# Kernel tuning notes

Hardware: AMD Instinct MI355X
Metric: run time of the kernel (lower is better)

## Reference

```python
import jax, jax.numpy as jnp
import numpy as np

N = 50000       # nodes
E = 800000      # directed edges (avg degree 16)
DIN, DH, DOUT = 128, 128, 64
NUM_LAYERS = 5


def setup_inputs() -> dict:
    key = jax.random.key(0)
    ks = jax.random.split(key, 2 + 2 * NUM_LAYERS)
    x = jax.random.normal(ks[0], (N, DIN), dtype=jnp.float32)
    edge_index = jax.random.randint(ks[1], (2, E), 0, N, dtype=jnp.int64)
    dims = [(DIN, DH)] + [(DH, DH)] * (NUM_LAYERS - 2) + [(DH, DOUT)]
    inp = {"x": x, "edge_index": edge_index}
    for i, (di, do) in enumerate(dims):
        # PyG Linear weight is [out, in]; glorot-ish scale
        inp[f"W{i}"] = jax.random.normal(ks[2 + 2 * i], (do, di), dtype=jnp.float32) / np.sqrt(di)
        inp[f"b{i}"] = jnp.zeros((do,), dtype=jnp.float32)
    return inp


def gcn_conv(x, W, b, src, dst, n):
    """PyG GCNConv: symmetric normalization with self-loops (already appended)."""
    h = x @ W.T                                   # [N, do]
    ones = jnp.ones(src.shape[0], dtype=h.dtype)
    deg = jax.ops.segment_sum(ones, dst, num_segments=n)          # [N]
    dinv = jnp.where(deg > 0, jax.lax.rsqrt(jnp.maximum(deg, 1.0)), 0.0)
    norm = dinv[src] * dinv[dst]                  # [E+N]
    msg = h[src] * norm[:, None]                  # [E+N, do] gather
    out = jax.ops.segment_sum(msg, dst, num_segments=n)           # scatter-add
    return out + b


def reference(x, edge_index, W0, b0, W1, b1, W2, b2, W3, b3, W4, b4):
    n = x.shape[0]
    loop = jnp.arange(n, dtype=edge_index.dtype)
    src = jnp.concatenate([edge_index[0], loop])  # add self-loops
    dst = jnp.concatenate([edge_index[1], loop])
    Ws = [W0, W1, W2, W3, W4]
    bs = [b0, b1, b2, b3, b4]
    for i in range(NUM_LAYERS):
        x = gcn_conv(x, Ws[i], bs[i], src, dst, n)
        if i != NUM_LAYERS - 1:
            x = jax.nn.relu(x)
            # dropout is identity in eval mode (training=False)
    return x
```

## Files before the change

### kernel.cpp

```cpp
#include <hip/hip_runtime.h>
#include <hip/hip_fp16.h>
#include <math.h>


typedef _Float16 f16x8 __attribute__((ext_vector_type(8)));
typedef float f32x4 __attribute__((ext_vector_type(4)));

#define NBIN 128
#define NB 512
#define WCAP 12288


__global__ __launch_bounds__(256) void k_detect(const int* __restrict__ ei, int* __restrict__ flag, int E) {
  __shared__ int nonzero;
  if (threadIdx.x == 0) nonzero = 0;
  __syncthreads();
  int idx = threadIdx.x;
  if (idx < E && idx < 256) {
    if (ei[2 * idx + 1] != 0) atomicOr(&nonzero, 1);
  }
  __syncthreads();
  if (threadIdx.x == 0) *flag = (nonzero == 0) ? 1 : 0;
}

__device__ __forceinline__ int edge_at(const void* ei, int is64, long long idx) {
  if (is64) return (int)((const long long*)ei)[idx];
  return ((const int*)ei)[idx];
}

__global__ __launch_bounds__(512) void k_cnt2(const void* __restrict__ ei, const int* __restrict__ flag,
                                              int* __restrict__ bcnt, int E, int n, int W) {
  __shared__ int cnt[NBIN];
  int t = threadIdx.x;
  if (t < NBIN) cnt[t] = 0;
  __syncthreads();
  int is64 = *flag;
  int chunk = (E + NB - 1) / NB;
  int base = blockIdx.x * chunk;
  int end = base + chunk;
  if (end > E) end = E;
  for (int i = base + t; i < end; i += 512) {
    int s = edge_at(ei, is64, i);
    int v = edge_at(ei, is64, (long long)E + i);
    if ((unsigned)v < (unsigned)n && (unsigned)s < (unsigned)n) atomicAdd(&cnt[v / W], 1);
  }
  __syncthreads();
  if (t < NBIN) bcnt[blockIdx.x * NBIN + t] = cnt[t];
}

__global__ __launch_bounds__(256) void k_scanb(int* __restrict__ bcnt, int* __restrict__ bintot) {
  __shared__ int buf[NB];
  int bin = blockIdx.x;
  int t = threadIdx.x;
  int a0 = bcnt[(size_t)t * NBIN + bin];
  int a1 = bcnt[(size_t)(t + 256) * NBIN + bin];
  buf[t] = a0;
  buf[t + 256] = a1;
  __syncthreads();
  for (int off = 1; off < NB; off <<= 1) {
    int x0 = (t >= off) ? buf[t - off] : 0;
    int x1 = (t + 256 >= off) ? buf[t + 256 - off] : 0;
    __syncthreads();
    buf[t] += x0;
    buf[t + 256] += x1;
    __syncthreads();
  }
  bcnt[(size_t)t * NBIN + bin] = buf[t] - a0;
  bcnt[(size_t)(t + 256) * NBIN + bin] = buf[t + 256] - a1;
  if (t == 255) bintot[bin] = buf[NB - 1];
}

__global__ __launch_bounds__(64) void k_base2(const int* __restrict__ bintot, int* __restrict__ binbase) {
  if (threadIdx.x == 0) {
    int run = 0;
    for (int i = 0; i < NBIN; ++i) {
      binbase[i] = run;
      run += bintot[i];
    }
    binbase[NBIN] = run;
  }
}

__global__ __launch_bounds__(512) void k_scat(const void* __restrict__ ei, const int* __restrict__ flag,
                                              const int* __restrict__ bcnt, const int* __restrict__ binbase,
                                              uint2* __restrict__ ebin, int E, int n, int W) {
  __shared__ int cur[NBIN];
  int t = threadIdx.x;
  if (t < NBIN) cur[t] = binbase[t] + bcnt[blockIdx.x * NBIN + t];
  __syncthreads();
  int is64 = *flag;
  int chunk = (E + NB - 1) / NB;
  int base = blockIdx.x * chunk;
  int end = base + chunk;
  if (end > E) end = E;
  for (int i = base + t; i < end; i += 512) {
    int s = edge_at(ei, is64, i);
    int v = edge_at(ei, is64, (long long)E + i);
    if ((unsigned)v < (unsigned)n && (unsigned)s < (unsigned)n) {
      int pos = atomicAdd(&cur[v / W], 1);
      ebin[pos] = make_uint2((unsigned)s, (unsigned)v);
    }
  }
}

__global__ __launch_bounds__(256) void k_build(const uint2* __restrict__ ebin, const int* __restrict__ binbase,
                                               int* __restrict__ row_ptr, float* __restrict__ dinv,
                                               int* __restrict__ col, int n, int W) {
  __shared__ int hist[512];
  __shared__ int scanBuf[512];
  __shared__ unsigned int win[WCAP];
  int t = threadIdx.x;
  int b = blockIdx.x;
  int v0 = b * W;
  int v1 = v0 + W;
  if (v1 > n) v1 = n;
  int nloc = v1 - v0;
  if (nloc <= 0) {
    if (b == NBIN - 1 && t == 0) row_ptr[n] = binbase[NBIN];
    return;
  }
  int ebase = binbase[b];
  int ecnt = binbase[b + 1] - ebase;

  for (int i = t; i < 512; i += 256) { hist[i] = 0; scanBuf[i] = 0; }
  __syncthreads();
  for (int j = t; j < ecnt; j += 256) {
    uint2 e = ebin[ebase + j];
    atomicAdd(&hist[(int)e.y - v0], 1);
  }
  __syncthreads();
  for (int i = t; i < nloc; i += 256) {
    scanBuf[i] = hist[i];
    dinv[v0 + i] = 1.0f / sqrtf((float)(hist[i] + 1));
  }
  __syncthreads();
  int i1 = t, i2 = t + 256;
  for (int off = 1; off < 512; off <<= 1) {
    int a = (i1 >= off) ? scanBuf[i1 - off] : 0;
    int c = (i2 >= off) ? scanBuf[i2 - off] : 0;
    __syncthreads();
    scanBuf[i1] += a;
    scanBuf[i2] += c;
    __syncthreads();
  }
  for (int i = t; i < nloc; i += 256) row_ptr[v0 + i] = ebase + scanBuf[i] - hist[i];
  if (b == NBIN - 1 && t == 0) row_ptr[n] = ebase + ecnt;
  __syncthreads();
  for (int i = t; i < nloc; i += 256) hist[i] = scanBuf[i] - hist[i];
  __syncthreads();
  if (ecnt <= WCAP) {
    for (int j = t; j < ecnt; j += 256) {
      uint2 e = ebin[ebase + j];
      int pos = atomicAdd(&hist[(int)e.y - v0], 1);
      win[pos] = e.x;
    }
    __syncthreads();
    for (int j = t; j < ecnt; j += 256) col[ebase + j] = (int)win[j];
  } else {
    for (int j = t; j < ecnt; j += 256) {
      uint2 e = ebin[ebase + j];
      int pos = atomicAdd(&hist[(int)e.y - v0], 1);
      col[ebase + pos] = (int)e.x;
    }
  }
}


__global__ __launch_bounds__(256) void k_split_x(const float* __restrict__ X, unsigned int* __restrict__ Xh,
                                                 unsigned int* __restrict__ Xr, int n2) {
  int i = blockIdx.x * 256 + threadIdx.x;
  if (i >= n2) return;
  float2 v = ((const float2*)X)[i];
  __half hx = __float2half(v.x), hy = __float2half(v.y);
  float rx = v.x - __half2float(hx), ry = v.y - __half2float(hy);
  __half rxh = __float2half(rx), ryh = __float2half(ry);
  unsigned int ph = ((unsigned int)*(unsigned short*)&hy << 16) | *(unsigned short*)&hx;
  unsigned int pr = ((unsigned int)*(unsigned short*)&ryh << 16) | *(unsigned short*)&rxh;
  Xh[i] = ph;
  Xr[i] = pr;
}

__global__ __launch_bounds__(256) void k_split_w(const float* __restrict__ W, unsigned short* __restrict__ Wh,
                                                 unsigned short* __restrict__ Wr, int cnt) {
  int i = blockIdx.x * 256 + threadIdx.x;
  if (i >= cnt) return;
  float v = W[i];
  __half h = __float2half(v);
  float r = v - __half2float(h);
  __half rh = __float2half(r);
  Wh[i] = *(unsigned short*)&h;
  Wr[i] = *(unsigned short*)&rh;
}


template <int DO>
__global__ __launch_bounds__(256) void gemm_mfma(const unsigned short* __restrict__ Xh,
                                                 const unsigned short* __restrict__ Xr,
                                                 const unsigned short* __restrict__ Wh,
                                                 const unsigned short* __restrict__ Wr,
                                                 const float* __restrict__ dinv, __half* __restrict__ G, int n) {
  constexpr int NCG = DO / 16;
  __shared__ unsigned short sWh[DO * 128];
  __shared__ unsigned short sWr[DO * 128];
  const int tid = threadIdx.x;

#pragma unroll
  for (int it = 0; it < DO / 16; ++it) {
    int t = it * 256 + tid;
    int row = t >> 4, ch = t & 15;
    int sch = ch ^ (row & 7);
    const uint4* gh = (const uint4*)&Wh[(size_t)t * 8];
    const uint4* gr = (const uint4*)&Wr[(size_t)t * 8];
    *(uint4*)&sWh[row * 128 + sch * 8] = *gh;
    *(uint4*)&sWr[row * 128 + sch * 8] = *gr;
  }

  const int wv = tid >> 6;
  const int l = tid & 63;
  const int m = l & 15;
  const int ks = l >> 4;
  const int gr0 = blockIdx.x * 64 + wv * 16;
  const int arow = gr0 + m;

  f16x8 ah[4], ar[4];
  const f16x8 z8 = {0, 0, 0, 0, 0, 0, 0, 0};
#pragma unroll
  for (int kb = 0; kb < 4; ++kb) {
    int koff = kb * 32 + ks * 8;
    if (arow < n) {
      ah[kb] = *(const f16x8*)&Xh[(size_t)arow * 128 + koff];
      ar[kb] = *(const f16x8*)&Xr[(size_t)arow * 128 + koff];
    } else {
      ah[kb] = z8;
      ar[kb] = z8;
    }
  }

  f32x4 acc[NCG];
#pragma unroll
  for (int c = 0; c < NCG; ++c) acc[c] = {0.f, 0.f, 0.f, 0.f};

  __syncthreads();

#pragma unroll
  for (int kb = 0; kb < 4; ++kb) {
    int ch = (kb * 4 + ks) ^ (m & 7);
#pragma unroll
    for (int c = 0; c < NCG; ++c) {
      int brow = c * 16 + m;
      f16x8 bh = *(const f16x8*)&sWh[brow * 128 + ch * 8];
      f16x8 br = *(const f16x8*)&sWr[brow * 128 + ch * 8];
      acc[c] = __builtin_amdgcn_mfma_f32_16x16x32_f16(ah[kb], bh, acc[c], 0, 0, 0);
      acc[c] = __builtin_amdgcn_mfma_f32_16x16x32_f16(ah[kb], br, acc[c], 0, 0, 0);
      acc[c] = __builtin_amdgcn_mfma_f32_16x16x32_f16(ar[kb], bh, acc[c], 0, 0, 0);
    }
  }

  int r0 = gr0 + ks * 4;
  float dv[4];
#pragma unroll
  for (int i = 0; i < 4; ++i) dv[i] = (r0 + i < n) ? dinv[r0 + i] : 0.f;
#pragma unroll
  for (int c = 0; c < NCG; ++c) {
#pragma unroll
    for (int i = 0; i < 4; ++i) {
      int row = r0 + i;
      if (row < n) G[(size_t)row * DO + c * 16 + m] = __float2half(dv[i] * acc[c][i]);
    }
  }
}


__device__ __forceinline__ float2 h2f(unsigned int u) {
  __half2 h = *(__half2*)&u;
  return __half22float2(h);
}

__global__ __launch_bounds__(256) void aggregate128(const unsigned int* __restrict__ G, const float* __restrict__ dinv,
                                                    const float* __restrict__ bias, const int* __restrict__ rp,
                                                    const int* __restrict__ col, unsigned int* __restrict__ Yh,
                                                    unsigned int* __restrict__ Yr, int n) {
  int v = (int)((blockIdx.x * 256 + threadIdx.x) >> 6);
  int lane = threadIdx.x & 63;
  if (v >= n) return;
  int s = rp[v], e = rp[v + 1];
  float2 a0 = h2f(G[(size_t)v * 64 + lane]);
  float2 a1 = make_float2(0.f, 0.f), a2 = make_float2(0.f, 0.f), a3 = make_float2(0.f, 0.f);
  int t = s;
  while (t < e) {
    int batch = e - t;
    if (batch > 64) batch = 64;
    int ci = col[t + (lane < batch ? lane : batch - 1)];
    int j = 0;
    for (; j + 4 <= batch; j += 4) {
      int u0 = __shfl(ci, j, 64), u1 = __shfl(ci, j + 1, 64);
      int u2 = __shfl(ci, j + 2, 64), u3 = __shfl(ci, j + 3, 64);
      float2 f0 = h2f(G[(size_t)u0 * 64 + lane]);
      float2 f1 = h2f(G[(size_t)u1 * 64 + lane]);
      float2 f2 = h2f(G[(size_t)u2 * 64 + lane]);
      float2 f3 = h2f(G[(size_t)u3 * 64 + lane]);
      a0.x += f0.x; a0.y += f0.y;
      a1.x += f1.x; a1.y += f1.y;
      a2.x += f2.x; a2.y += f2.y;
      a3.x += f3.x; a3.y += f3.y;
    }
    for (; j < batch; ++j) {
      int u = __shfl(ci, j, 64);
      float2 f = h2f(G[(size_t)u * 64 + lane]);
      a0.x += f.x; a0.y += f.y;
    }
    t += batch;
  }
  float sx = (a0.x + a1.x) + (a2.x + a3.x);
  float sy = (a0.y + a1.y) + (a2.y + a3.y);
  float dv = dinv[v];
  float2 bb = ((const float2*)bias)[lane];
  float ox = fmaxf(fmaf(dv, sx, bb.x), 0.f);
  float oy = fmaxf(fmaf(dv, sy, bb.y), 0.f);
  __half hx = __float2half(ox), hy = __float2half(oy);
  float rx = ox - __half2float(hx), ry = oy - __half2float(hy);
  __half rxh = __float2half(rx), ryh = __float2half(ry);
  size_t o = (size_t)v * 64 + lane;
  Yh[o] = ((unsigned int)*(unsigned short*)&hy << 16) | *(unsigned short*)&hx;
  Yr[o] = ((unsigned int)*(unsigned short*)&ryh << 16) | *(unsigned short*)&rxh;
}

__global__ __launch_bounds__(256) void aggregate64(const unsigned short* __restrict__ G, const float* __restrict__ dinv,
                                                   const float* __restrict__ bias, const int* __restrict__ rp,
                                                   const int* __restrict__ col, float* __restrict__ Y, int n) {
  int v = (int)((blockIdx.x * 256 + threadIdx.x) >> 6);
  int lane = threadIdx.x & 63;
  if (v >= n) return;
  int s = rp[v], e = rp[v + 1];
  float a0 = __half2float(*(const __half*)&G[(size_t)v * 64 + lane]);
  float a1 = 0.f, a2 = 0.f, a3 = 0.f;
  int t = s;
  while (t < e) {
    int batch = e - t;
    if (batch > 64) batch = 64;
    int ci = col[t + (lane < batch ? lane : batch - 1)];
    int j = 0;
    for (; j + 4 <= batch; j += 4) {
      int u0 = __shfl(ci, j, 64), u1 = __shfl(ci, j + 1, 64);
      int u2 = __shfl(ci, j + 2, 64), u3 = __shfl(ci, j + 3, 64);
      unsigned short g0 = G[(size_t)u0 * 64 + lane];
      unsigned short g1 = G[(size_t)u1 * 64 + lane];
      unsigned short g2 = G[(size_t)u2 * 64 + lane];
      unsigned short g3 = G[(size_t)u3 * 64 + lane];
      a0 += __half2float(*(const __half*)&g0);
      a1 += __half2float(*(const __half*)&g1);
      a2 += __half2float(*(const __half*)&g2);
      a3 += __half2float(*(const __half*)&g3);
    }
    for (; j < batch; ++j) {
      int u = __shfl(ci, j, 64);
      unsigned short g = G[(size_t)u * 64 + lane];
      a0 += __half2float(*(const __half*)&g);
    }
    t += batch;
  }
  float sum = (a0 + a1) + (a2 + a3);
  Y[(size_t)v * 64 + lane] = fmaf(dinv[v], sum, bias[lane]);
}


extern "C" void kernel_launch(void* const* d_in, const int* in_sizes, int n_in,
                              void* d_out, int out_size, void* d_ws, size_t ws_size,
                              hipStream_t stream) {
  const float* x = (const float*)d_in[0];
  const void* ei = d_in[1];
  const int N = in_sizes[0] / 128;
  const int E = in_sizes[1] / 2;
  const float* W[5] = {(const float*)d_in[2], (const float*)d_in[4], (const float*)d_in[6],
                       (const float*)d_in[8], (const float*)d_in[10]};
  const float* B[5] = {(const float*)d_in[3], (const float*)d_in[5], (const float*)d_in[7],
                       (const float*)d_in[9], (const float*)d_in[11]};
  const int wcnt[5] = {128 * 128, 128 * 128, 128 * 128, 128 * 128, 64 * 128};
  const int Wbin = (N + NBIN - 1) / NBIN;

  char* p = (char*)d_ws;
  unsigned short* xyh = (unsigned short*)p;  p += (size_t)N * 128 * 2;
  unsigned short* xyr = (unsigned short*)p;  p += (size_t)N * 128 * 2;
  __half* g = (__half*)p;                    p += (size_t)N * 128 * 2;
  uint2* ebin = (uint2*)g;
  unsigned short* wh = (unsigned short*)p;   p += (size_t)5 * 16384 * 2;
  unsigned short* wr = (unsigned short*)p;   p += (size_t)5 * 16384 * 2;
  float* dinv = (float*)p;                   p += (size_t)N * 4;
  int* col = (int*)p;                        p += (size_t)E * 4;
  int* row_ptr = (int*)p;                    p += (size_t)(N + 1) * 4;
  int* bcnt = (int*)p;                       p += (size_t)NB * NBIN * 4;
  int* bintot = (int*)p;                     p += NBIN * 4;
  int* binbase = (int*)p;                    p += (NBIN + 1) * 4;
  int* flag = (int*)p;                       p += 16;

  k_detect<<<1, 256, 0, stream>>>((const int*)ei, flag, E);
  k_cnt2<<<NB, 512, 0, stream>>>(ei, flag, bcnt, E, N, Wbin);
  k_scanb<<<NBIN, 256, 0, stream>>>(bcnt, bintot);
  k_base2<<<1, 64, 0, stream>>>(bintot, binbase);
  k_scat<<<NB, 512, 0, stream>>>(ei, flag, bcnt, binbase, ebin, E, N, Wbin);
  k_build<<<NBIN, 256, 0, stream>>>(ebin, binbase, row_ptr, dinv, col, N, Wbin);

  k_split_x<<<(N * 64 + 255) / 256, 256, 0, stream>>>(x, (unsigned int*)xyh, (unsigned int*)xyr, N * 64);
  for (int l = 0; l < 5; ++l)
    k_split_w<<<(wcnt[l] + 255) / 256, 256, 0, stream>>>(W[l], wh + l * 16384, wr + l * 16384, wcnt[l]);

  const int gb = (N + 63) / 64;
  const int ab = (N * 64 + 255) / 256;

  for (int l = 0; l < 4; ++l) {
    gemm_mfma<128><<<gb, 256, 0, stream>>>(xyh, xyr, wh + l * 16384, wr + l * 16384, dinv, g, N);
    aggregate128<<<ab, 256, 0, stream>>>((const unsigned int*)g, dinv, B[l], row_ptr, col,
                                         (unsigned int*)xyh, (unsigned int*)xyr, N);
  }
  gemm_mfma<64><<<gb, 256, 0, stream>>>(xyh, xyr, wh + 4 * 16384, wr + 4 * 16384, dinv, g, N);
  aggregate64<<<ab, 256, 0, stream>>>((const unsigned short*)g, dinv, B[4], row_ptr, col, (float*)d_out, N);
}
```

Baseline: 312.6 us.

## Fold setup kernels together and split 128-wide aggregation into column chunks

The int64 detection moves into the count and scatter kernels, and the bin-base prefix scan is recomputed inside the scatter and build kernels. This removes the separate detect and base kernels, and the five per-layer weight-split launches are merged into one. The 128-wide aggregation now gives each block a 16-column-pair chunk over 32 nodes, with four lane groups each taking a different neighbour and a shuffle reduction at the end. That aims at more parallelism and better cache locality for the gather, at the cost of redundant col reads and a 4x larger grid.

Result: slower. 534.0 us (+70.8%).

```diff
diff --git a/kernel.cpp b/kernel.cpp
--- a/kernel.cpp
+++ b/kernel.cpp
@@ -11,30 +11,30 @@
 #define WCAP 12288
 
 
-__global__ __launch_bounds__(256) void k_detect(const int* __restrict__ ei, int* __restrict__ flag, int E) {
-  __shared__ int nonzero;
-  if (threadIdx.x == 0) nonzero = 0;
-  __syncthreads();
-  int idx = threadIdx.x;
-  if (idx < E && idx < 256) {
-    if (ei[2 * idx + 1] != 0) atomicOr(&nonzero, 1);
-  }
-  __syncthreads();
-  if (threadIdx.x == 0) *flag = (nonzero == 0) ? 1 : 0;
-}
-
 __device__ __forceinline__ int edge_at(const void* ei, int is64, long long idx) {
   if (is64) return (int)((const long long*)ei)[idx];
   return ((const int*)ei)[idx];
 }
 
-__global__ __launch_bounds__(512) void k_cnt2(const void* __restrict__ ei, const int* __restrict__ flag,
-                                              int* __restrict__ bcnt, int E, int n, int W) {
+__device__ __forceinline__ int detect_is64(const int* ei32, int E, int* ldsflag, int tid) {
+  if (tid == 0) *ldsflag = 0;
+  __syncthreads();
+  int lim = (E < 256) ? E : 256;
+  if (tid < lim) {
+    if (ei32[2 * tid + 1] != 0) atomicOr(ldsflag, 1);
+  }
+  __syncthreads();
+  return (*ldsflag == 0) ? 1 : 0;
+}
+
+__global__ __launch_bounds__(512) void k_cnt2(const void* __restrict__ ei, int* __restrict__ bcnt,
+                                              int E, int n, int W) {
   __shared__ int cnt[NBIN];
+  __shared__ int f64;
   int t = threadIdx.x;
+  int is64 = detect_is64((const int*)ei, E, &f64, t);
   if (t < NBIN) cnt[t] = 0;
   __syncthreads();
-  int is64 = *flag;
   int chunk = (E + NB - 1) / NB;
   int base = blockIdx.x * chunk;
   int end = base + chunk;
@@ -70,25 +70,25 @@
   if (t == 255) bintot[bin] = buf[NB - 1];
 }
 
-__global__ __launch_bounds__(64) void k_base2(const int* __restrict__ bintot, int* __restrict__ binbase) {
-  if (threadIdx.x == 0) {
-    int run = 0;
-    for (int i = 0; i < NBIN; ++i) {
-      binbase[i] = run;
-      run += bintot[i];
-    }
-    binbase[NBIN] = run;
-  }
-}
-
-__global__ __launch_bounds__(512) void k_scat(const void* __restrict__ ei, const int* __restrict__ flag,
-                                              const int* __restrict__ bcnt, const int* __restrict__ binbase,
-                                              uint2* __restrict__ ebin, int E, int n, int W) {
+__global__ __launch_bounds__(512) void k_scat(const void* __restrict__ ei, const int* __restrict__ bintot,
+                                              const int* __restrict__ bcnt, uint2* __restrict__ ebin,
+                                              int E, int n, int W) {
+  __shared__ int f64;
+  __shared__ int sb[NBIN];
   __shared__ int cur[NBIN];
   int t = threadIdx.x;
-  if (t < NBIN) cur[t] = binbase[t] + bcnt[blockIdx.x * NBIN + t];
-  __syncthreads();
-  int is64 = *flag;
+  int is64 = detect_is64((const int*)ei, E, &f64, t);
+  if (t < NBIN) sb[t] = bintot[t];
+  __syncthreads();
+  for (int off = 1; off < NBIN; off <<= 1) {
+    int x = 0;
+    if (t < NBIN && t >= off) x = sb[t - off];
+    __syncthreads();
+    if (t < NBIN) sb[t] += x;
+    __syncthreads();
+  }
+  if (t < NBIN) cur[t] = sb[t] - bintot[t] + bcnt[blockIdx.x * NBIN + t];
+  __syncthreads();
   int chunk = (E + NB - 1) / NB;
   int base = blockIdx.x * chunk;
   int end = base + chunk;
@@ -103,24 +103,36 @@
   }
 }
 
-__global__ __launch_bounds__(256) void k_build(const uint2* __restrict__ ebin, const int* __restrict__ binbase,
+__global__ __launch_bounds__(256) void k_build(const uint2* __restrict__ ebin, const int* __restrict__ bintot,
                                                int* __restrict__ row_ptr, float* __restrict__ dinv,
                                                int* __restrict__ col, int n, int W) {
   __shared__ int hist[512];
   __shared__ int scanBuf[512];
+  __shared__ int sb[NBIN];
   __shared__ unsigned int win[WCAP];
   int t = threadIdx.x;
   int b = blockIdx.x;
+  if (t < NBIN) sb[t] = bintot[t];
+  __syncthreads();
+  for (int off = 1; off < NBIN; off <<= 1) {
+    int x = 0;
+    if (t < NBIN && t >= off) x = sb[t - off];
+    __syncthreads();
+    if (t < NBIN) sb[t] += x;
+    __syncthreads();
+  }
+  int ebase = sb[b] - bintot[b];
+  int ecnt = bintot[b];
+  int etotal = sb[NBIN - 1];
+
   int v0 = b * W;
   int v1 = v0 + W;
   if (v1 > n) v1 = n;
   int nloc = v1 - v0;
   if (nloc <= 0) {
-    if (b == NBIN - 1 && t == 0) row_ptr[n] = binbase[NBIN];
+    if (b == NBIN - 1 && t == 0) row_ptr[n] = etotal;
     return;
   }
-  int ebase = binbase[b];
-  int ecnt = binbase[b + 1] - ebase;
 
   for (int i = t; i < 512; i += 256) { hist[i] = 0; scanBuf[i] = 0; }
   __syncthreads();
@@ -144,7 +156,7 @@
     __syncthreads();
   }
   for (int i = t; i < nloc; i += 256) row_ptr[v0 + i] = ebase + scanBuf[i] - hist[i];
-  if (b == NBIN - 1 && t == 0) row_ptr[n] = ebase + ecnt;
+  if (b == NBIN - 1 && t == 0) row_ptr[n] = etotal;
   __syncthreads();
   for (int i = t; i < nloc; i += 256) hist[i] = scanBuf[i] - hist[i];
   __syncthreads();
@@ -174,17 +186,27 @@
   __half hx = __float2half(v.x), hy = __float2half(v.y);
   float rx = v.x - __half2float(hx), ry = v.y - __half2float(hy);
   __half rxh = __float2half(rx), ryh = __float2half(ry);
-  unsigned int ph = ((unsigned int)*(unsigned short*)&hy << 16) | *(unsigned short*)&hx;
-  unsigned int pr = ((unsigned int)*(unsigned short*)&ryh << 16) | *(unsigned short*)&rxh;
-  Xh[i] = ph;
-  Xr[i] = pr;
-}
-
-__global__ __launch_bounds__(256) void k_split_w(const float* __restrict__ W, unsigned short* __restrict__ Wh,
-                                                 unsigned short* __restrict__ Wr, int cnt) {
+  Xh[i] = ((unsigned int)*(unsigned short*)&hy << 16) | *(unsigned short*)&hx;
+  Xr[i] = ((unsigned int)*(unsigned short*)&ryh << 16) | *(unsigned short*)&rxh;
+}
+
+__global__ __launch_bounds__(256) void k_split_wall(const float* __restrict__ W0, const float* __restrict__ W1,
+                                                    const float* __restrict__ W2, const float* __restrict__ W3,
+                                                    const float* __restrict__ W4, unsigned short* __restrict__ Wh,
+                                                    unsigned short* __restrict__ Wr, int total) {
   int i = blockIdx.x * 256 + threadIdx.x;
-  if (i >= cnt) return;
-  float v = W[i];
+  if (i >= total) return;
+  const float* src;
+  int off;
+  if (i < 65536) {
+    int l = i >> 14;
+    off = i & 16383;
+    src = (l == 0) ? W0 : (l == 1) ? W1 : (l == 2) ? W2 : W3;
+  } else {
+    off = i - 65536;
+    src = W4;
+  }
+  float v = src[off];
   __half h = __float2half(v);
   float r = v - __half2float(h);
   __half rh = __float2half(r);
@@ -276,53 +298,56 @@
   return __half22float2(h);
 }
 
-__global__ __launch_bounds__(256) void aggregate128(const unsigned int* __restrict__ G, const float* __restrict__ dinv,
-                                                    const float* __restrict__ bias, const int* __restrict__ rp,
-                                                    const int* __restrict__ col, unsigned int* __restrict__ Yh,
-                                                    unsigned int* __restrict__ Yr, int n) {
-  int v = (int)((blockIdx.x * 256 + threadIdx.x) >> 6);
-  int lane = threadIdx.x & 63;
-  if (v >= n) return;
-  int s = rp[v], e = rp[v + 1];
-  float2 a0 = h2f(G[(size_t)v * 64 + lane]);
-  float2 a1 = make_float2(0.f, 0.f), a2 = make_float2(0.f, 0.f), a3 = make_float2(0.f, 0.f);
-  int t = s;
-  while (t < e) {
-    int batch = e - t;
-    if (batch > 64) batch = 64;
-    int ci = col[t + (lane < batch ? lane : batch - 1)];
-    int j = 0;
-    for (; j + 4 <= batch; j += 4) {
-      int u0 = __shfl(ci, j, 64), u1 = __shfl(ci, j + 1, 64);
-      int u2 = __shfl(ci, j + 2, 64), u3 = __shfl(ci, j + 3, 64);
-      float2 f0 = h2f(G[(size_t)u0 * 64 + lane]);
-      float2 f1 = h2f(G[(size_t)u1 * 64 + lane]);
-      float2 f2 = h2f(G[(size_t)u2 * 64 + lane]);
-      float2 f3 = h2f(G[(size_t)u3 * 64 + lane]);
-      a0.x += f0.x; a0.y += f0.y;
-      a1.x += f1.x; a1.y += f1.y;
-      a2.x += f2.x; a2.y += f2.y;
-      a3.x += f3.x; a3.y += f3.y;
-    }
-    for (; j < batch; ++j) {
-      int u = __shfl(ci, j, 64);
-      float2 f = h2f(G[(size_t)u * 64 + lane]);
-      a0.x += f.x; a0.y += f.y;
-    }
-    t += batch;
-  }
-  float sx = (a0.x + a1.x) + (a2.x + a3.x);
-  float sy = (a0.y + a1.y) + (a2.y + a3.y);
-  float dv = dinv[v];
-  float2 bb = ((const float2*)bias)[lane];
-  float ox = fmaxf(fmaf(dv, sx, bb.x), 0.f);
-  float oy = fmaxf(fmaf(dv, sy, bb.y), 0.f);
-  __half hx = __float2half(ox), hy = __float2half(oy);
-  float rx = ox - __half2float(hx), ry = oy - __half2float(hy);
-  __half rxh = __float2half(rx), ryh = __float2half(ry);
-  size_t o = (size_t)v * 64 + lane;
-  Yh[o] = ((unsigned int)*(unsigned short*)&hy << 16) | *(unsigned short*)&hx;
-  Yr[o] = ((unsigned int)*(unsigned short*)&ryh << 16) | *(unsigned short*)&rxh;
+__global__ __launch_bounds__(256) void aggregate128c(const unsigned int* __restrict__ G,
+                                                     const float* __restrict__ dinv,
+                                                     const float* __restrict__ bias, const int* __restrict__ rp,
+                                                     const int* __restrict__ col, unsigned int* __restrict__ Yh,
+                                                     unsigned int* __restrict__ Yr, int n) {
+  const int c = blockIdx.x & 3;
+  const int tile = blockIdx.x >> 2;
+  const int wv = threadIdx.x >> 6, lane = threadIdx.x & 63;
+  const int q = lane >> 4, r = lane & 15;
+  const int co = c * 16 + r;
+  const int vbase = tile * 32 + wv * 8;
+  for (int k = 0; k < 8; ++k) {
+    int v = vbase + k;
+    if (v >= n) break;
+    int s = rp[v], e = rp[v + 1];
+    float2 acc = make_float2(0.f, 0.f);
+    if (q == 0) acc = h2f(G[(size_t)v * 64 + co]);
+    int t = s;
+    while (t < e) {
+      int batch = e - t;
+      if (batch > 64) batch = 64;
+      int ci = col[t + (lane < batch ? lane : batch - 1)];
+      for (int j = 0; j < batch; j += 4) {
+        int jq = j + q;
+        int u = __shfl(ci, jq < batch ? jq : batch - 1, 64);
+        if (jq < batch) {
+          float2 f = h2f(G[(size_t)u * 64 + co]);
+          acc.x += f.x;
+          acc.y += f.y;
+        }
+      }
+      t += batch;
+    }
+    acc.x += __shfl_xor(acc.x, 16, 64);
+    acc.y += __shfl_xor(acc.y, 16, 64);
+    acc.x += __shfl_xor(acc.x, 32, 64);
+    acc.y += __shfl_xor(acc.y, 32, 64);
+    if (q == 0) {
+      float dv = dinv[v];
+      float2 bb = ((const float2*)bias)[co];
+      float ox = fmaxf(fmaf(dv, acc.x, bb.x), 0.f);
+      float oy = fmaxf(fmaf(dv, acc.y, bb.y), 0.f);
+      __half hx = __float2half(ox), hy = __float2half(oy);
+      float rx = ox - __half2float(hx), ry = oy - __half2float(hy);
+      __half rxh = __float2half(rx), ryh = __float2half(ry);
+      size_t o = (size_t)v * 64 + co;
+      Yh[o] = ((unsigned int)*(unsigned short*)&hy << 16) | *(unsigned short*)&hx;
+      Yr[o] = ((unsigned int)*(unsigned short*)&ryh << 16) | *(unsigned short*)&rxh;
+    }
+  }
 }
 
 __global__ __launch_bounds__(256) void aggregate64(const unsigned short* __restrict__ G, const float* __restrict__ dinv,
@@ -375,7 +400,6 @@
                        (const float*)d_in[8], (const float*)d_in[10]};
   const float* B[5] = {(const float*)d_in[3], (const float*)d_in[5], (const float*)d_in[7],
                        (const float*)d_in[9], (const float*)d_in[11]};
-  const int wcnt[5] = {128 * 128, 128 * 128, 128 * 128, 128 * 128, 64 * 128};
   const int Wbin = (N + NBIN - 1) / NBIN;
 
   char* p = (char*)d_ws;
@@ -390,27 +414,23 @@
   int* row_ptr = (int*)p;                    p += (size_t)(N + 1) * 4;
   int* bcnt = (int*)p;                       p += (size_t)NB * NBIN * 4;
   int* bintot = (int*)p;                     p += NBIN * 4;
-  int* binbase = (int*)p;                    p += (NBIN + 1) * 4;
-  int* flag = (int*)p;                       p += 16;
-
-  k_detect<<<1, 256, 0, stream>>>((const int*)ei, flag, E);
-  k_cnt2<<<NB, 512, 0, stream>>>(ei, flag, bcnt, E, N, Wbin);
+
+  k_cnt2<<<NB, 512, 0, stream>>>(ei, bcnt, E, N, Wbin);
   k_scanb<<<NBIN, 256, 0, stream>>>(bcnt, bintot);
-  k_base2<<<1, 64, 0, stream>>>(bintot, binbase);
-  k_scat<<<NB, 512, 0, stream>>>(ei, flag, bcnt, binbase, ebin, E, N, Wbin);
-  k_build<<<NBIN, 256, 0, stream>>>(ebin, binbase, row_ptr, dinv, col, N, Wbin);
+  k_scat<<<NB, 512, 0, stream>>>(ei, bintot, bcnt, ebin, E, N, Wbin);
+  k_build<<<NBIN, 256, 0, stream>>>(ebin, bintot, row_ptr, dinv, col, N, Wbin);
 
   k_split_x<<<(N * 64 + 255) / 256, 256, 0, stream>>>(x, (unsigned int*)xyh, (unsigned int*)xyr, N * 64);
-  for (int l = 0; l < 5; ++l)
-    k_split_w<<<(wcnt[l] + 255) / 256, 256, 0, stream>>>(W[l], wh + l * 16384, wr + l * 16384, wcnt[l]);
+  k_split_wall<<<(73728 + 255) / 256, 256, 0, stream>>>(W[0], W[1], W[2], W[3], W[4], wh, wr, 73728);
 
   const int gb = (N + 63) / 64;
+  const int acb = 4 * ((N + 31) / 32);
   const int ab = (N * 64 + 255) / 256;
 
   for (int l = 0; l < 4; ++l) {
     gemm_mfma<128><<<gb, 256, 0, stream>>>(xyh, xyr, wh + l * 16384, wr + l * 16384, dinv, g, N);
-    aggregate128<<<ab, 256, 0, stream>>>((const unsigned int*)g, dinv, B[l], row_ptr, col,
-                                         (unsigned int*)xyh, (unsigned int*)xyr, N);
+    aggregate128c<<<acb, 256, 0, stream>>>((const unsigned int*)g, dinv, B[l], row_ptr, col,
+                                           (unsigned int*)xyh, (unsigned int*)xyr, N);
   }
   gemm_mfma<64><<<gb, 256, 0, stream>>>(xyh, xyr, wh + 4 * 16384, wr + 4 * 16384, dinv, g, N);
   aggregate64<<<ab, 256, 0, stream>>>((const unsigned short*)g, dinv, B[4], row_ptr, col, (float*)d_out, N);
```
